# Kernel optimization log

Hardware: AMD Instinct MI355X
Metric: run time of the kernel (lower is better)

## Reference

```python
import jax, jax.numpy as jnp
import numpy as np

DIM = 512; HEADS = 8; DH = 64; CHUNK = 64; DHID = DH * 4; MAX_LR = 1.0; EPS = 1e-6


def rmsnorm(x, w):
    return x * jax.lax.rsqrt(jnp.mean(x * x, axis=-1, keepdims=True) + EPS) * w


def mem_forward(params, x):
    # MemoryMLP(depth=2, expansion=4) wrapped in ResidualNorm
    nw, w0, w1 = params
    h = rmsnorm(x, nw)
    y = jax.nn.gelu(h @ w0) @ w1
    return y + x


def chunk_loss(params, k, lr, v):
    pred = mem_forward(params, k)            # (CHUNK, DH)
    loss = jnp.mean((pred - v) ** 2, axis=-1)  # per-token mse, (CHUNK,)
    return (loss * lr).sum(), loss


def assoc_scan(gates, inputs, prev=None):
    # h_t = g_t * h_{t-1} + x_t along axis=1 (chunks)
    def combine(a, b):
        g1, x1 = a; g2, x2 = b
        return g1 * g2, x2 + g2 * x1
    G, X = jax.lax.associative_scan(combine, (gates, inputs), axis=1)
    if prev is None:
        return X
    return X + G * prev[:, None]


def setup_inputs() -> dict:
    key = jax.random.key(0)
    ks = jax.random.split(key, 8)
    B, N = 2, 4096
    s = 0.02
    return {
        'seq': jax.random.normal(ks[0], (B, N, DIM), jnp.float32),
        'store_norm_w': jnp.ones((DIM,), jnp.float32),
        'Wk': jax.random.normal(ks[1], (DIM, HEADS * DH), jnp.float32) * s,
        'Wv': jax.random.normal(ks[2], (DIM, HEADS * DH), jnp.float32) * s,
        'Wstep': jax.random.normal(ks[3], (DIM, HEADS), jnp.float32) * s,
        'bstep': jnp.zeros((HEADS,), jnp.float32),
        'Wmom': jax.random.normal(ks[4], (DIM, HEADS), jnp.float32) * s,
        'bmom': jnp.zeros((HEADS,), jnp.float32),
        'Wdec': jax.random.normal(ks[5], (DIM, HEADS), jnp.float32) * s,
        'bdec': jnp.zeros((HEADS,), jnp.float32),
        'mem_norm_w': jnp.ones((HEADS, DH), jnp.float32),
        'mem_w0': jax.random.normal(ks[6], (HEADS, DH, DHID), jnp.float32) * s,
        'mem_w1': jax.random.normal(ks[7], (HEADS, DHID, DH), jnp.float32) * s,
    }


def reference(seq, store_norm_w, Wk, Wv, Wstep, bstep, Wmom, bmom, Wdec, bdec, mem_norm_w, mem_w0, mem_w1):
    B, N, _ = seq.shape
    nc = N // CHUNK
    bh = B * HEADS
    x = rmsnorm(seq, store_norm_w)                        # store pre-norm, (B,N,D)
    # per-token adaptive lr: 'b n h -> (b h) n', sigmoid * max_lr
    lr = jax.nn.sigmoid(x @ Wstep + bstep) * MAX_LR       # (B,N,H)
    lr = lr.transpose(0, 2, 1).reshape(bh, nc, CHUNK)
    # chunk-pooled rep (AveragePool) -> momentum / decay gates per chunk
    pooled = x.reshape(B, nc, CHUNK, DIM).mean(axis=2)    # (B,nc,D)
    mom = jax.nn.sigmoid(pooled @ Wmom + bmom).transpose(0, 2, 1).reshape(bh, nc, 1)
    decay = jax.nn.sigmoid(pooled @ Wdec + bdec).transpose(0, 2, 1).reshape(bh, nc, 1)

    def split(t):  # (B,N,H*DH) -> (bh, nc, CHUNK, DH)
        return t.reshape(B, N, HEADS, DH).transpose(0, 2, 1, 3).reshape(bh, nc, CHUNK, DH)
    k = split(x @ Wk)
    v = split(x @ Wv)

    # initial fast weights per (b h) stream: repeat 'h ... -> (b h) ...'
    params0 = (jnp.tile(mem_norm_w, (B, 1)),
               jnp.tile(mem_w0, (B, 1, 1)),
               jnp.tile(mem_w1, (B, 1, 1)))

    # per-chunk per-stream grads via vmap(grad) (all chunks share the initial weights)
    grad_fn = jax.grad(chunk_loss, has_aux=True)
    per_chunk = jax.vmap(grad_fn, in_axes=(None, 0, 0, 0))
    per_bh = jax.vmap(per_chunk, in_axes=(0, 0, 0, 0))
    grads, _ = per_bh(params0, k, lr, v)                  # tuple of (bh, nc, *shape)

    finals = []
    for g, w0 in zip(grads, params0):
        surprise = -g
        extra = (1,) * (g.ndim - 2)
        m = mom.reshape(bh, nc, *extra)
        d = decay.reshape(bh, nc, *extra)
        update = assoc_scan(m, surprise)                  # momentum scan, zero init
        wts = assoc_scan(1.0 - d, update, prev=w0)        # decay recurrence from init weights
        finals.append(wts[:, -1].reshape(bh, -1))
    return jnp.concatenate(finals, axis=-1)              # (bh, DH + DH*DHID + DHID*DH)
```

## Files before the change

kernel.cpp:

```cpp
#include <hip/hip_runtime.h>
#include <math.h>

typedef __attribute__((ext_vector_type(8)))  __bf16 bf16x8;
typedef __attribute__((ext_vector_type(4)))  float  f32x4;
typedef __attribute__((ext_vector_type(4)))  unsigned short ushort4v;
typedef __attribute__((ext_vector_type(8)))  unsigned short ushort8v;

#define MFMA16(acc, a, b) acc = __builtin_amdgcn_mfma_f32_16x16x32_bf16((a),(b),(acc),0,0,0)

__device__ inline unsigned short f2b(float f) {
    union { float f; unsigned int u; } v; v.f = f;
    unsigned int r = v.u + 0x7FFFu + ((v.u >> 16) & 1u);
    return (unsigned short)(r >> 16);
}
__device__ inline float b2f(unsigned short h) {
    union { unsigned int u; float f; } v; v.u = ((unsigned int)h) << 16;
    return v.f;
}
__device__ inline float tanh_fast(float z) {
    float e = __expf(2.0f * z);
    return 1.0f - 2.0f / (e + 1.0f);
}
__device__ inline float gelu_g(float x) {
    const float c0 = 0.7978845608028654f, c1 = 0.044715f;
    float z = c0 * x * (1.0f + c1 * x * x);
    return 0.5f * x * (1.0f + tanh_fast(z));
}
__device__ inline void gelu_both(float x, float& g, float& gp) {
    const float c0 = 0.7978845608028654f, c1 = 0.044715f;
    float x2 = x * x;
    float z  = c0 * x * (1.0f + c1 * x2);
    float t  = tanh_fast(z);
    g  = 0.5f * x * (1.0f + t);
    float dz = c0 * (1.0f + 3.0f * c1 * x2);
    gp = 0.5f * (1.0f + t) + 0.5f * x * (1.0f - t * t) * dz;
}
__device__ inline float sigmoidf(float x) { return 1.0f / (1.0f + __expf(-x)); }

__global__ __launch_bounds__(256) void k_wprep(
    const float* __restrict__ Wk, const float* __restrict__ Wv,
    const float* __restrict__ w0_g, const float* __restrict__ w1_g,
    const float* __restrict__ nw_g,
    unsigned short* __restrict__ WkvT, unsigned short* __restrict__ w0fT,
    unsigned short* __restrict__ w1T, unsigned short* __restrict__ w0N,
    unsigned short* __restrict__ w1N)
{
    const int bid = blockIdx.x, tid = threadIdx.x;
    __shared__ float tile[64][65];
    if (bid < 128) {
        int kt = bid >> 4, nt = bid & 15;
        const float* src = (nt < 8) ? Wk : Wv;
        int ncol0 = (nt & 7) * 64;
        for (int ii = 0; ii < 16; ++ii) {
            int idx = tid + ii * 256; int r = idx >> 6, cc = idx & 63;
            tile[r][cc] = src[(size_t)(kt * 64 + r) * 512 + ncol0 + cc];
        }
        __syncthreads();
        for (int ii = 0; ii < 16; ++ii) {
            int idx = tid + ii * 256; int r = idx >> 6, cc = idx & 63;
            WkvT[(size_t)(nt * 64 + r) * 512 + kt * 64 + cc] = f2b(tile[cc][r]);
        }
    } else if (bid < 160) {
        int q = bid - 128; int hh = q >> 2, it = q & 3;
        const float* w0h = w0_g + hh * 16384;
        for (int ii = 0; ii < 16; ++ii) {
            int idx = tid + ii * 256; int r = idx >> 6, cc = idx & 63;
            tile[r][cc] = w0h[r * 256 + it * 64 + cc];
        }
        __syncthreads();
        for (int ii = 0; ii < 16; ++ii) {
            int idx = tid + ii * 256; int r = idx >> 6, cc = idx & 63;
            w0fT[hh * 16384 + (it * 64 + r) * 64 + cc] = f2b(nw_g[hh * 64 + cc] * tile[cc][r]);
        }
    } else if (bid < 192) {
        int q = bid - 160; int hh = q >> 2, it = q & 3;
        const float* w1h = w1_g + hh * 16384;
        for (int ii = 0; ii < 16; ++ii) {
            int idx = tid + ii * 256; int r = idx >> 6, cc = idx & 63;
            tile[r][cc] = w1h[(it * 64 + r) * 64 + cc];
        }
        __syncthreads();
        for (int ii = 0; ii < 16; ++ii) {
            int idx = tid + ii * 256; int r = idx >> 6, cc = idx & 63;
            w1T[hh * 16384 + r * 256 + it * 64 + cc] = f2b(tile[cc][r]);
        }
    } else {
        int q = bid - 192;
        int gid = q * 2048 + tid * 8;
        const float* s; unsigned short* d;
        if (gid < 131072) { s = w0_g + gid; d = w0N + gid; }
        else              { s = w1_g + (gid - 131072); d = w1N + (gid - 131072); }
        #pragma unroll
        for (int jj = 0; jj < 8; ++jj) d[jj] = f2b(s[jj]);
    }
}

__global__ __launch_bounds__(256) void k_rms_lr(
    const float* __restrict__ seq, const float* __restrict__ wnorm,
    const float* __restrict__ Wstep, const float* __restrict__ bstep,
    unsigned short* __restrict__ xb, float* __restrict__ lrb)
{
    const int wid = threadIdx.x >> 6, lane = threadIdx.x & 63;
    const int t = blockIdx.x * 4 + wid;
    const float* row = seq + (size_t)t * 512 + lane * 8;
    float v[8];
    *(f32x4*)&v[0] = *(const f32x4*)row;
    *(f32x4*)&v[4] = *(const f32x4*)(row + 4);
    float ss = 0.f;
    #pragma unroll
    for (int j = 0; j < 8; ++j) ss += v[j] * v[j];
    #pragma unroll
    for (int o = 1; o < 64; o <<= 1) ss += __shfl_xor(ss, o);
    float rr = rsqrtf(ss * (1.0f / 512.0f) + 1e-6f);
    const float* wn = wnorm + lane * 8;
    ushort8v xs;
    float acc[8] = {0.f,0.f,0.f,0.f,0.f,0.f,0.f,0.f};
    #pragma unroll
    for (int j = 0; j < 8; ++j) {
        float xf = v[j] * rr * wn[j];
        xs[j] = f2b(xf);
        const float* wrow = Wstep + (size_t)(lane * 8 + j) * 8;
        #pragma unroll
        for (int h = 0; h < 8; ++h) acc[h] = fmaf(xf, wrow[h], acc[h]);
    }
    *(ushort8v*)(xb + (size_t)t * 512 + lane * 8) = xs;
    #pragma unroll
    for (int h = 0; h < 8; ++h) {
        #pragma unroll
        for (int o = 1; o < 64; o <<= 1) acc[h] += __shfl_xor(acc[h], o);
    }
    if (lane == 0) {
        #pragma unroll
        for (int h = 0; h < 8; ++h) lrb[(size_t)t * 8 + h] = sigmoidf(acc[h] + bstep[h]);
    }
}

__global__ __launch_bounds__(256) void k_pool(
    const unsigned short* __restrict__ xb, float* __restrict__ pooled)
{
    __shared__ float sP[4][512];
    const int bc = blockIdx.x, tid = threadIdx.x;
    const int q = tid >> 6, lane = tid & 63, d0 = lane * 8;
    float p[8] = {0.f,0.f,0.f,0.f,0.f,0.f,0.f,0.f};
    for (int tt = 0; tt < 16; ++tt) {
        int t = q * 16 + tt;
        ushort8v v = *(const ushort8v*)(xb + (size_t)(bc * 64 + t) * 512 + d0);
        #pragma unroll
        for (int j = 0; j < 8; ++j) p[j] += b2f(v[j]);
    }
    #pragma unroll
    for (int j = 0; j < 8; ++j) sP[q][d0 + j] = p[j];
    __syncthreads();
    #pragma unroll
    for (int half = 0; half < 2; ++half) {
        int d = tid + half * 256;
        pooled[(size_t)bc * 512 + d] =
            (sP[0][d] + sP[1][d] + sP[2][d] + sP[3][d]) * (1.0f / 64.0f);
    }
}

__global__ __launch_bounds__(256) void k_proj(
    const unsigned short* __restrict__ xb, const unsigned short* __restrict__ WkvT,
    unsigned short* __restrict__ kbh, unsigned short* __restrict__ vb)
{
    __shared__ __attribute__((aligned(16))) unsigned short As[128][72];
    __shared__ __attribute__((aligned(16))) unsigned short Bs[128][72];
    const int tid = threadIdx.x;
    const int bm = blockIdx.x >> 3, bn = blockIdx.x & 7;
    const int m0 = bm * 128, n0 = bn * 128;
    const int wid = tid >> 6, lane = tid & 63, lg = lane >> 4, lo = lane & 15;
    const int wm = wid >> 1, wn = wid & 1;
    f32x4 acc[4][4];
    #pragma unroll
    for (int i = 0; i < 4; ++i)
        #pragma unroll
        for (int j = 0; j < 4; ++j) acc[i][j] = (f32x4)0.f;

    for (int k0 = 0; k0 < 512; k0 += 64) {
        #pragma unroll
        for (int ii = 0; ii < 4; ++ii) {
            int e0 = tid * 32 + ii * 8;
            int r = e0 >> 6, c = e0 & 63;
            *(bf16x8*)&As[r][c] = *(const bf16x8*)(xb   + (size_t)(m0 + r) * 512 + k0 + c);
            *(bf16x8*)&Bs[r][c] = *(const bf16x8*)(WkvT + (size_t)(n0 + r) * 512 + k0 + c);
        }
        __syncthreads();
        #pragma unroll
        for (int ks = 0; ks < 2; ++ks) {
            bf16x8 aF[4], bF[4];
            #pragma unroll
            for (int mt = 0; mt < 4; ++mt) aF[mt] = *(const bf16x8*)&As[wm * 64 + mt * 16 + lo][ks * 32 + 8 * lg];
            #pragma unroll
            for (int nt = 0; nt < 4; ++nt) bF[nt] = *(const bf16x8*)&Bs[wn * 64 + nt * 16 + lo][ks * 32 + 8 * lg];
            #pragma unroll
            for (int mt = 0; mt < 4; ++mt)
                #pragma unroll
                for (int nt = 0; nt < 4; ++nt) MFMA16(acc[mt][nt], aF[mt], bF[nt]);
        }
        __syncthreads();
    }
    #pragma unroll
    for (int mt = 0; mt < 4; ++mt)
        #pragma unroll
        for (int nt = 0; nt < 4; ++nt)
            #pragma unroll
            for (int r = 0; r < 4; ++r) {
                int row = m0 + wm * 64 + mt * 16 + lg * 4 + r;
                int col = n0 + wn * 64 + nt * 16 + lo;
                unsigned short val = f2b(acc[mt][nt][r]);
                if (col < 512) kbh[(size_t)row * 512 + col] = val;
                else           vb[(size_t)row * 512 + col - 512] = val;
            }
}

__global__ __launch_bounds__(64) void k_gates(
    const float* __restrict__ pooled,
    const float* __restrict__ Wmom, const float* __restrict__ bmom,
    const float* __restrict__ Wdec, const float* __restrict__ bdec,
    float* __restrict__ momout, float* __restrict__ decout)
{
    const int bc = blockIdx.x;
    const int tid = threadIdx.x, h = tid & 7, d0 = tid >> 3;
    const float* pr = pooled + (size_t)bc * 512;
    float pm = 0.f, pd = 0.f;
    #pragma unroll 8
    for (int it = 0; it < 64; ++it) {
        int d = d0 + it * 8; float pv = pr[d];
        pm = fmaf(pv, Wmom[d * 8 + h], pm);
        pd = fmaf(pv, Wdec[d * 8 + h], pd);
    }
    #pragma unroll
    for (int o = 8; o < 64; o <<= 1) { pm += __shfl_xor(pm, o); pd += __shfl_xor(pd, o); }
    if (tid < 8) {
        momout[(size_t)bc * 8 + h] = sigmoidf(pm + bmom[h]);
        decout[(size_t)bc * 8 + h] = sigmoidf(pd + bdec[h]);
    }
}

__global__ void k_coeff(const float* __restrict__ mom, const float* __restrict__ dec,
                        float* __restrict__ coeff, float* __restrict__ Aout)
{
    int s = threadIdx.x;
    if (s >= 16) return;
    int b = s >> 3, h = s & 7;
    float P = 1.f, S = 1.f;
    coeff[s * 64 + 63] = 1.f;
    for (int cc = 62; cc >= 0; --cc) {
        float Dn = 1.f - dec[(size_t)(b * 64 + cc + 1) * 8 + h];
        float Mn = mom[(size_t)(b * 64 + cc + 1) * 8 + h];
        P *= Dn;
        S = P + Mn * S;
        coeff[s * 64 + cc] = S;
    }
    float D0 = 1.f - dec[(size_t)(b * 64) * 8 + h];
    Aout[s] = P * D0;
}

__global__ __launch_bounds__(256) void k_fwd(
    const unsigned short* __restrict__ kbh, const unsigned short* __restrict__ vb,
    const float* __restrict__ lrb, const float* __restrict__ cfb,
    const unsigned short* __restrict__ w0fT, const unsigned short* __restrict__ w1T,
    unsigned short* __restrict__ uws, unsigned short* __restrict__ ews,
    unsigned short* __restrict__ ewsT)
{
    __shared__ __attribute__((aligned(16))) unsigned short sU[64][72];
    __shared__ __attribute__((aligned(16))) unsigned short sG[64][72];
    const int tid = threadIdx.x, blk = blockIdx.x;
    const int s = blk >> 6, c = blk & 63;
    const int b = s >> 3, h = s & 7;
    const int row0 = b * 4096 + c * 64;
    const int wid = tid >> 6, lane = tid & 63, lg = lane >> 4, lo = lane & 15;
    const size_t ubase = (size_t)blk * 4096;

    for (int tt = 0; tt < 16; ++tt) {
        int t = wid * 16 + tt;
        float kv = b2f(kbh[(size_t)(row0 + t) * 512 + h * 64 + lane]);
        float ss = kv * kv;
        #pragma unroll
        for (int o = 1; o < 64; o <<= 1) ss += __shfl_xor(ss, o);
        float rr = rsqrtf(ss * (1.0f / 64.0f) + 1e-6f);
        sU[t][lane] = f2b(kv * rr);
    }
    __syncthreads();
    {
        int r = tid >> 2, c0 = (tid & 3) * 16;
        *(ushort8v*)(uws + ubase + r * 64 + c0)     = *(const ushort8v*)&sU[r][c0];
        *(ushort8v*)(uws + ubase + r * 64 + c0 + 8) = *(const ushort8v*)&sU[r][c0 + 8];
    }

    const unsigned short* w0h = w0fT + h * 16384;
    const unsigned short* w1h = w1T  + h * 16384;
    bf16x8 aF0 = *(const bf16x8*)&sU[wid * 16 + lo][8 * lg];
    bf16x8 aF1 = *(const bf16x8*)&sU[wid * 16 + lo][32 + 8 * lg];

    f32x4 yac[4];
    #pragma unroll
    for (int nt = 0; nt < 4; ++nt) yac[nt] = (f32x4)0.f;

    for (int is = 0; is < 4; ++is) {
        f32x4 a1[4];
        #pragma unroll
        for (int nt = 0; nt < 4; ++nt) a1[nt] = (f32x4)0.f;
        #pragma unroll
        for (int nt = 0; nt < 4; ++nt) {
            bf16x8 b0 = *(const bf16x8*)(w0h + (size_t)(is * 64 + nt * 16 + lo) * 64 + 8 * lg);
            bf16x8 b1 = *(const bf16x8*)(w0h + (size_t)(is * 64 + nt * 16 + lo) * 64 + 32 + 8 * lg);
            MFMA16(a1[nt], aF0, b0);
            MFMA16(a1[nt], aF1, b1);
        }
        if (is > 0) __syncthreads();
        #pragma unroll
        for (int nt = 0; nt < 4; ++nt)
            #pragma unroll
            for (int r = 0; r < 4; ++r) {
                int t = wid * 16 + lg * 4 + r;
                sG[t][nt * 16 + lo] = f2b(gelu_g(a1[nt][r]));
            }
        __syncthreads();
        #pragma unroll
        for (int ks = 0; ks < 2; ++ks) {
            bf16x8 aW = *(const bf16x8*)(w1h + (size_t)(wid * 16 + lo) * 256 + is * 64 + ks * 32 + 8 * lg);
            #pragma unroll
            for (int nt = 0; nt < 4; ++nt) {
                bf16x8 bG = *(const bf16x8*)&sG[nt * 16 + lo][ks * 32 + 8 * lg];
                MFMA16(yac[nt], aW, bG);
            }
        }
    }

    float coefv = cfb[s * 64 + c];
    ushort4v evs[4];
    #pragma unroll
    for (int nt = 0; nt < 4; ++nt) {
        int t = nt * 16 + lo; int grow = row0 + t;
        float sc = -coefv * lrb[(size_t)grow * 8 + h] * (2.0f / 64.0f);
        ushort4v k4 = *(const ushort4v*)(kbh + (size_t)grow * 512 + h * 64 + wid * 16 + lg * 4);
        ushort4v v4 = *(const ushort4v*)(vb  + (size_t)grow * 512 + h * 64 + wid * 16 + lg * 4);
        ushort4v ev;
        #pragma unroll
        for (int r = 0; r < 4; ++r)
            ev[r] = f2b(sc * (yac[nt][r] + b2f(k4[r]) - b2f(v4[r])));
        evs[nt] = ev;
        *(ushort4v*)(ews + ubase + t * 64 + wid * 16 + lg * 4) = ev;
    }

    __syncthreads();
    #pragma unroll
    for (int nt = 0; nt < 4; ++nt)
        *(ushort4v*)&sG[nt * 16 + lo][wid * 16 + lg * 4] = evs[nt];
    __syncthreads();
    {
        int r2 = tid >> 2, c2 = (tid & 3) * 16;
        ushort8v o0, o1;
        #pragma unroll
        for (int jj = 0; jj < 8; ++jj) o0[jj] = sG[c2 + jj][r2];
        #pragma unroll
        for (int jj = 0; jj < 8; ++jj) o1[jj] = sG[c2 + 8 + jj][r2];
        *(ushort8v*)(ewsT + ubase + r2 * 64 + c2)     = o0;
        *(ushort8v*)(ewsT + ubase + r2 * 64 + c2 + 8) = o1;
    }
}

__global__ __launch_bounds__(256) void k_bwd(
    const unsigned short* __restrict__ uws, const unsigned short* __restrict__ ews,
    const unsigned short* __restrict__ ewsT,
    const unsigned short* __restrict__ w0fT, const unsigned short* __restrict__ w0N,
    const unsigned short* __restrict__ w1N, const float* __restrict__ nw_g,
    float* __restrict__ pws, float* __restrict__ gnwb)
{
    __shared__ __attribute__((aligned(16))) unsigned short sGT[64][72];
    __shared__ __attribute__((aligned(16))) unsigned short sDAT[64][72];
    __shared__ __attribute__((aligned(16))) unsigned short sDAN[64][68];
    const int tid = threadIdx.x, blk = blockIdx.x;
    const int s = blk >> 5, ksl = (blk >> 2) & 7, is = blk & 3;
    const int h = s & 7;
    const int wid = tid >> 6, lane = tid & 63, lg = lane >> 4, lo = lane & 15;

    f32x4 gw1a[4], gw0a[4];
    #pragma unroll
    for (int nt = 0; nt < 4; ++nt) { gw1a[nt] = (f32x4)0.f; gw0a[nt] = (f32x4)0.f; }
    float gnwp[4] = {0.f, 0.f, 0.f, 0.f};

    const unsigned short* w0fh = w0fT + h * 16384;
    const unsigned short* w0nh = w0N  + h * 16384;
    const unsigned short* w1nh = w1N  + h * 16384;

    for (int tt = 0; tt < 8; ++tt) {
        __syncthreads();
        const int chunk = ksl * 8 + tt;
        const size_t base = (size_t)(s * 64 + chunk) * 4096;

        unsigned short utg[16];
        #pragma unroll
        for (int ks = 0; ks < 2; ++ks)
            #pragma unroll
            for (int jj = 0; jj < 8; ++jj)
                utg[ks * 8 + jj] = uws[base + (size_t)(ks * 32 + 8 * lg + jj) * 64 + wid * 16 + lo];

        f32x4 a1[4];
        #pragma unroll
        for (int nt = 0; nt < 4; ++nt) a1[nt] = (f32x4)0.f;
        bf16x8 aF0 = *(const bf16x8*)(uws + base + (size_t)(wid * 16 + lo) * 64 + 8 * lg);
        bf16x8 aF1 = *(const bf16x8*)(uws + base + (size_t)(wid * 16 + lo) * 64 + 32 + 8 * lg);
        #pragma unroll
        for (int nt = 0; nt < 4; ++nt) {
            bf16x8 b0 = *(const bf16x8*)(w0fh + (size_t)(is * 64 + nt * 16 + lo) * 64 + 8 * lg);
            bf16x8 b1 = *(const bf16x8*)(w0fh + (size_t)(is * 64 + nt * 16 + lo) * 64 + 32 + 8 * lg);
            MFMA16(a1[nt], aF0, b0);
            MFMA16(a1[nt], aF1, b1);
        }
        float gpv[4][4];
        #pragma unroll
        for (int nt = 0; nt < 4; ++nt) {
            ushort4v gv;
            #pragma unroll
            for (int r = 0; r < 4; ++r) {
                float g, gp; gelu_both(a1[nt][r], g, gp);
                gv[r] = f2b(g); gpv[nt][r] = gp;
            }
            *(ushort4v*)&sGT[nt * 16 + lo][wid * 16 + lg * 4] = gv;
        }

        f32x4 dga[4];
        #pragma unroll
        for (int nt = 0; nt < 4; ++nt) dga[nt] = (f32x4)0.f;
        bf16x8 eF0 = *(const bf16x8*)(ews + base + (size_t)(wid * 16 + lo) * 64 + 8 * lg);
        bf16x8 eF1 = *(const bf16x8*)(ews + base + (size_t)(wid * 16 + lo) * 64 + 32 + 8 * lg);
        #pragma unroll
        for (int nt = 0; nt < 4; ++nt) {
            bf16x8 b0 = *(const bf16x8*)(w1nh + (size_t)(is * 64 + nt * 16 + lo) * 64 + 8 * lg);
            bf16x8 b1 = *(const bf16x8*)(w1nh + (size_t)(is * 64 + nt * 16 + lo) * 64 + 32 + 8 * lg);
            MFMA16(dga[nt], eF0, b0);
            MFMA16(dga[nt], eF1, b1);
        }
        #pragma unroll
        for (int nt = 0; nt < 4; ++nt) {
            ushort4v dv;
            #pragma unroll
            for (int r = 0; r < 4; ++r) dv[r] = f2b(dga[nt][r] * gpv[nt][r]);
            *(ushort4v*)&sDAT[nt * 16 + lo][wid * 16 + lg * 4] = dv;
            #pragma unroll
            for (int r = 0; r < 4; ++r) sDAN[wid * 16 + lg * 4 + r][nt * 16 + lo] = dv[r];
        }
        __syncthreads();

        #pragma unroll
        for (int ks = 0; ks < 2; ++ks) {
            bf16x8 aG = *(const bf16x8*)&sGT[wid * 16 + lo][ks * 32 + 8 * lg];
            #pragma unroll
            for (int nt = 0; nt < 4; ++nt) {
                bf16x8 bE = *(const bf16x8*)(ewsT + base + (size_t)(nt * 16 + lo) * 64 + ks * 32 + 8 * lg);
                MFMA16(gw1a[nt], aG, bE);
            }
        }
        #pragma unroll
        for (int ks = 0; ks < 2; ++ks) {
            union { ushort8v u; bf16x8 b; } cu;
            #pragma unroll
            for (int jj = 0; jj < 8; ++jj) cu.u[jj] = utg[ks * 8 + jj];
            #pragma unroll
            for (int nt = 0; nt < 4; ++nt) {
                bf16x8 bD = *(const bf16x8*)&sDAT[nt * 16 + lo][ks * 32 + 8 * lg];
                MFMA16(gw0a[nt], cu.b, bD);
            }
        }
        f32x4 dht[4];
        #pragma unroll
        for (int nt = 0; nt < 4; ++nt) dht[nt] = (f32x4)0.f;
        #pragma unroll
        for (int ks = 0; ks < 2; ++ks) {
            bf16x8 aW0 = *(const bf16x8*)(w0nh + (size_t)(wid * 16 + lo) * 256 + is * 64 + ks * 32 + 8 * lg);
            #pragma unroll
            for (int nt = 0; nt < 4; ++nt) {
                bf16x8 bDA = *(const bf16x8*)&sDAN[nt * 16 + lo][ks * 32 + 8 * lg];
                MFMA16(dht[nt], aW0, bDA);
            }
        }
        #pragma unroll
        for (int nt = 0; nt < 4; ++nt) {
            ushort4v u4 = *(const ushort4v*)(uws + base + (size_t)(nt * 16 + lo) * 64 + wid * 16 + lg * 4);
            #pragma unroll
            for (int r = 0; r < 4; ++r)
                gnwp[r] += b2f(u4[r]) * dht[nt][r];
        }
    }

    size_t pb = (size_t)blk * 8192;
    #pragma unroll
    for (int nt = 0; nt < 4; ++nt)
        #pragma unroll
        for (int r = 0; r < 4; ++r)
            pws[pb + (size_t)(wid * 16 + lg * 4 + r) * 64 + nt * 16 + lo] = gw1a[nt][r];
    #pragma unroll
    for (int r = 0; r < 4; ++r) {
        float nwv = nw_g[h * 64 + wid * 16 + lg * 4 + r];
        #pragma unroll
        for (int nt = 0; nt < 4; ++nt)
            pws[pb + 4096 + (size_t)(wid * 16 + lg * 4 + r) * 64 + nt * 16 + lo] = nwv * gw0a[nt][r];
    }
    #pragma unroll
    for (int r = 0; r < 4; ++r) {
        #pragma unroll
        for (int o = 1; o < 16; o <<= 1) gnwp[r] += __shfl_xor(gnwp[r], o);
    }
    if (lo == 0) {
        #pragma unroll
        for (int r = 0; r < 4; ++r)
            gnwb[(size_t)blk * 64 + wid * 16 + lg * 4 + r] = gnwp[r];
    }
}

__global__ __launch_bounds__(256) void k_reduce(
    const float* __restrict__ pws, const float* __restrict__ gnwb,
    const float* __restrict__ Ab,
    const float* __restrict__ nw_g, const float* __restrict__ w0_g,
    const float* __restrict__ w1_g, float* __restrict__ out)
{
    int gid = blockIdx.x * 256 + threadIdx.x;
    if (gid >= 16 * 32832) return;
    int s = gid / 32832, r = gid % 32832;
    int h = s & 7;
    float A = Ab[s];
    float val;
    if (r < 64) {
        val = A * nw_g[h * 64 + r];
        #pragma unroll
        for (int ks = 0; ks < 8; ++ks)
            #pragma unroll
            for (int i2 = 0; i2 < 4; ++i2)
                val += gnwb[(size_t)(s * 32 + ks * 4 + i2) * 64 + r];
    } else if (r < 16448) {
        int rr = r - 64; int d = rr >> 8; int i = rr & 255; int i2 = i >> 6, iloc = i & 63;
        val = A * w0_g[h * 16384 + rr];
        #pragma unroll
        for (int ks = 0; ks < 8; ++ks)
            val += pws[(size_t)(s * 32 + ks * 4 + i2) * 8192 + 4096 + d * 64 + iloc];
    } else {
        int rr = r - 16448; int i = rr >> 6; int j = rr & 63; int i2 = i >> 6, iloc = i & 63;
        val = A * w1_g[h * 16384 + rr];
        #pragma unroll
        for (int ks = 0; ks < 8; ++ks)
            val += pws[(size_t)(s * 32 + ks * 4 + i2) * 8192 + iloc * 64 + j];
    }
    out[gid] = val;
}

extern "C" void kernel_launch(void* const* d_in, const int* in_sizes, int n_in,
                              void* d_out, int out_size, void* d_ws, size_t ws_size,
                              hipStream_t stream) {
    (void)in_sizes; (void)n_in; (void)out_size; (void)ws_size;
    const float* seq   = (const float*)d_in[0];
    const float* snw   = (const float*)d_in[1];
    const float* Wk    = (const float*)d_in[2];
    const float* Wv    = (const float*)d_in[3];
    const float* Wstep = (const float*)d_in[4];
    const float* bstep = (const float*)d_in[5];
    const float* Wmom  = (const float*)d_in[6];
    const float* bmom  = (const float*)d_in[7];
    const float* Wdec  = (const float*)d_in[8];
    const float* bdec  = (const float*)d_in[9];
    const float* nw_g  = (const float*)d_in[10];
    const float* w0_g  = (const float*)d_in[11];
    const float* w1_g  = (const float*)d_in[12];
    float* out = (float*)d_out;

    char* ws = (char*)d_ws;
    unsigned short* xb   = (unsigned short*)(ws + 0);
    unsigned short* uws  = (unsigned short*)(ws + 0);
    unsigned short* WkvT = (unsigned short*)(ws + 8388608);
    float*          gnwb = (float*)        (ws + 8388608);
    unsigned short* kbh  = (unsigned short*)(ws + 9437184);
    unsigned short* vb   = (unsigned short*)(ws + 17825792);
    float*          pws  = (float*)        (ws + 9437184);
    unsigned short* ews  = (unsigned short*)(ws + 26214400);
    unsigned short* ewsT = (unsigned short*)(ws + 34603008);
    unsigned short* w0fT = (unsigned short*)(ws + 42991616);
    unsigned short* w1T  = (unsigned short*)(ws + 43253760);
    unsigned short* w0N  = (unsigned short*)(ws + 43515904);
    unsigned short* w1N  = (unsigned short*)(ws + 43778048);
    float* lrb  = (float*)(ws + 44040192);
    float* plb  = (float*)(ws + 44302336);
    float* momb = (float*)(ws + 44564480);
    float* decb = (float*)(ws + 44568576);
    float* cfb  = (float*)(ws + 44572672);
    float* Ab   = (float*)(ws + 44576768);

    k_wprep <<<320, 256, 0, stream>>>(Wk, Wv, w0_g, w1_g, nw_g, WkvT, w0fT, w1T, w0N, w1N);
    k_rms_lr<<<2048, 256, 0, stream>>>(seq, snw, Wstep, bstep, xb, lrb);
    k_pool  <<<128, 256, 0, stream>>>(xb, plb);
    k_proj  <<<512, 256, 0, stream>>>(xb, WkvT, kbh, vb);
    k_gates <<<128, 64, 0, stream>>>(plb, Wmom, bmom, Wdec, bdec, momb, decb);
    k_coeff <<<1, 64, 0, stream>>>(momb, decb, cfb, Ab);
    k_fwd   <<<1024, 256, 0, stream>>>(kbh, vb, lrb, cfb, w0fT, w1T, uws, ews, ewsT);
    k_bwd   <<<512, 256, 0, stream>>>(uws, ews, ewsT, w0fT, w0N, w1N, nw_g, pws, gnwb);
    k_reduce<<<2052, 256, 0, stream>>>(pws, gnwb, Ab, nw_g, w0_g, w1_g, out);
}
```

Before: 152.5 us.

## Replace partial-sum reduce kernel with atomic accumulation and split backward finer

After: 177.8 us. +16.6%, slower.

```diff
diff --git a/kernel.cpp b/kernel.cpp
--- a/kernel.cpp
+++ b/kernel.cpp
@@ -256,6 +256,22 @@
     Aout[s] = P * D0;
 }
 
+__global__ __launch_bounds__(256) void k_init_out(
+    const float* __restrict__ nw_g, const float* __restrict__ w0_g,
+    const float* __restrict__ w1_g, const float* __restrict__ Aout,
+    float* __restrict__ out)
+{
+    int gid = blockIdx.x * 256 + threadIdx.x;
+    if (gid >= 16 * 32832) return;
+    int s = gid / 32832, r = gid % 32832;
+    int h = s & 7;
+    float v;
+    if (r < 64)          v = nw_g[h * 64 + r];
+    else if (r < 16448)  v = w0_g[h * 16384 + (r - 64)];
+    else                 v = w1_g[h * 16384 + (r - 16448)];
+    out[gid] = Aout[s] * v;
+}
+
 __global__ __launch_bounds__(256) void k_fwd(
     const unsigned short* __restrict__ kbh, const unsigned short* __restrict__ vb,
     const float* __restrict__ lrb, const float* __restrict__ cfb,
@@ -272,21 +288,29 @@
     const int wid = tid >> 6, lane = tid & 63, lg = lane >> 4, lo = lane & 15;
     const size_t ubase = (size_t)blk * 4096;
 
-    for (int tt = 0; tt < 16; ++tt) {
-        int t = wid * 16 + tt;
-        float kv = b2f(kbh[(size_t)(row0 + t) * 512 + h * 64 + lane]);
-        float ss = kv * kv;
-        #pragma unroll
-        for (int o = 1; o < 64; o <<= 1) ss += __shfl_xor(ss, o);
-        float rr = rsqrtf(ss * (1.0f / 64.0f) + 1e-6f);
-        sU[t][lane] = f2b(kv * rr);
-    }
-    __syncthreads();
     {
         int r = tid >> 2, c0 = (tid & 3) * 16;
-        *(ushort8v*)(uws + ubase + r * 64 + c0)     = *(const ushort8v*)&sU[r][c0];
-        *(ushort8v*)(uws + ubase + r * 64 + c0 + 8) = *(const ushort8v*)&sU[r][c0 + 8];
-    }
+        const unsigned short* kr = kbh + (size_t)(row0 + r) * 512 + h * 64 + c0;
+        ushort8v k0 = *(const ushort8v*)kr;
+        ushort8v k1 = *(const ushort8v*)(kr + 8);
+        float kv[16];
+        float ss = 0.f;
+        #pragma unroll
+        for (int j = 0; j < 8; ++j) { kv[j] = b2f(k0[j]); kv[8 + j] = b2f(k1[j]); }
+        #pragma unroll
+        for (int j = 0; j < 16; ++j) ss += kv[j] * kv[j];
+        ss += __shfl_xor(ss, 1);
+        ss += __shfl_xor(ss, 2);
+        float rr = rsqrtf(ss * (1.0f / 64.0f) + 1e-6f);
+        ushort8v u0, u1;
+        #pragma unroll
+        for (int j = 0; j < 8; ++j) { u0[j] = f2b(kv[j] * rr); u1[j] = f2b(kv[8 + j] * rr); }
+        *(ushort8v*)&sU[r][c0]     = u0;
+        *(ushort8v*)&sU[r][c0 + 8] = u1;
+        *(ushort8v*)(uws + ubase + r * 64 + c0)     = u0;
+        *(ushort8v*)(uws + ubase + r * 64 + c0 + 8) = u1;
+    }
+    __syncthreads();
 
     const unsigned short* w0h = w0fT + h * 16384;
     const unsigned short* w1h = w1T  + h * 16384;
@@ -366,13 +390,13 @@
     const unsigned short* __restrict__ ewsT,
     const unsigned short* __restrict__ w0fT, const unsigned short* __restrict__ w0N,
     const unsigned short* __restrict__ w1N, const float* __restrict__ nw_g,
-    float* __restrict__ pws, float* __restrict__ gnwb)
+    float* __restrict__ out)
 {
     __shared__ __attribute__((aligned(16))) unsigned short sGT[64][72];
     __shared__ __attribute__((aligned(16))) unsigned short sDAT[64][72];
     __shared__ __attribute__((aligned(16))) unsigned short sDAN[64][68];
     const int tid = threadIdx.x, blk = blockIdx.x;
-    const int s = blk >> 5, ksl = (blk >> 2) & 7, is = blk & 3;
+    const int s = blk >> 6, ksl = (blk >> 2) & 15, is = blk & 3;
     const int h = s & 7;
     const int wid = tid >> 6, lane = tid & 63, lg = lane >> 4, lo = lane & 15;
 
@@ -385,9 +409,9 @@
     const unsigned short* w0nh = w0N  + h * 16384;
     const unsigned short* w1nh = w1N  + h * 16384;
 
-    for (int tt = 0; tt < 8; ++tt) {
-        __syncthreads();
-        const int chunk = ksl * 8 + tt;
+    for (int tt = 0; tt < 4; ++tt) {
+        __syncthreads();
+        const int chunk = ksl * 4 + tt;
         const size_t base = (size_t)(s * 64 + chunk) * 4096;
 
         unsigned short utg[16];
@@ -485,64 +509,32 @@
         }
     }
 
-    size_t pb = (size_t)blk * 8192;
+    float* outS = out + (size_t)s * 32832;
     #pragma unroll
     for (int nt = 0; nt < 4; ++nt)
         #pragma unroll
+        for (int r = 0; r < 4; ++r) {
+            int iglob = is * 64 + wid * 16 + lg * 4 + r;
+            atomicAdd(outS + 16448 + iglob * 64 + nt * 16 + lo, gw1a[nt][r]);
+        }
+    #pragma unroll
+    for (int r = 0; r < 4; ++r) {
+        int d = wid * 16 + lg * 4 + r;
+        float nwv = nw_g[h * 64 + d];
+        #pragma unroll
+        for (int nt = 0; nt < 4; ++nt)
+            atomicAdd(outS + 64 + d * 256 + is * 64 + nt * 16 + lo, nwv * gw0a[nt][r]);
+    }
+    #pragma unroll
+    for (int r = 0; r < 4; ++r) {
+        #pragma unroll
+        for (int o = 1; o < 16; o <<= 1) gnwp[r] += __shfl_xor(gnwp[r], o);
+    }
+    if (lo == 0) {
+        #pragma unroll
         for (int r = 0; r < 4; ++r)
-            pws[pb + (size_t)(wid * 16 + lg * 4 + r) * 64 + nt * 16 + lo] = gw1a[nt][r];
-    #pragma unroll
-    for (int r = 0; r < 4; ++r) {
-        float nwv = nw_g[h * 64 + wid * 16 + lg * 4 + r];
-        #pragma unroll
-        for (int nt = 0; nt < 4; ++nt)
-            pws[pb + 4096 + (size_t)(wid * 16 + lg * 4 + r) * 64 + nt * 16 + lo] = nwv * gw0a[nt][r];
-    }
-    #pragma unroll
-    for (int r = 0; r < 4; ++r) {
-        #pragma unroll
-        for (int o = 1; o < 16; o <<= 1) gnwp[r] += __shfl_xor(gnwp[r], o);
-    }
-    if (lo == 0) {
-        #pragma unroll
-        for (int r = 0; r < 4; ++r)
-            gnwb[(size_t)blk * 64 + wid * 16 + lg * 4 + r] = gnwp[r];
-    }
-}
-
-__global__ __launch_bounds__(256) void k_reduce(
-    const float* __restrict__ pws, const float* __restrict__ gnwb,
-    const float* __restrict__ Ab,
-    const float* __restrict__ nw_g, const float* __restrict__ w0_g,
-    const float* __restrict__ w1_g, float* __restrict__ out)
-{
-    int gid = blockIdx.x * 256 + threadIdx.x;
-    if (gid >= 16 * 32832) return;
-    int s = gid / 32832, r = gid % 32832;
-    int h = s & 7;
-    float A = Ab[s];
-    float val;
-    if (r < 64) {
-        val = A * nw_g[h * 64 + r];
-        #pragma unroll
-        for (int ks = 0; ks < 8; ++ks)
-            #pragma unroll
-            for (int i2 = 0; i2 < 4; ++i2)
-                val += gnwb[(size_t)(s * 32 + ks * 4 + i2) * 64 + r];
-    } else if (r < 16448) {
-        int rr = r - 64; int d = rr >> 8; int i = rr & 255; int i2 = i >> 6, iloc = i & 63;
-        val = A * w0_g[h * 16384 + rr];
-        #pragma unroll
-        for (int ks = 0; ks < 8; ++ks)
-            val += pws[(size_t)(s * 32 + ks * 4 + i2) * 8192 + 4096 + d * 64 + iloc];
-    } else {
-        int rr = r - 16448; int i = rr >> 6; int j = rr & 63; int i2 = i >> 6, iloc = i & 63;
-        val = A * w1_g[h * 16384 + rr];
-        #pragma unroll
-        for (int ks = 0; ks < 8; ++ks)
-            val += pws[(size_t)(s * 32 + ks * 4 + i2) * 8192 + iloc * 64 + j];
-    }
-    out[gid] = val;
+            atomicAdd(outS + wid * 16 + lg * 4 + r, gnwp[r]);
+    }
 }
 
 extern "C" void kernel_launch(void* const* d_in, const int* in_sizes, int n_in,
@@ -568,10 +560,8 @@
     unsigned short* xb   = (unsigned short*)(ws + 0);
     unsigned short* uws  = (unsigned short*)(ws + 0);
     unsigned short* WkvT = (unsigned short*)(ws + 8388608);
-    float*          gnwb = (float*)        (ws + 8388608);
     unsigned short* kbh  = (unsigned short*)(ws + 9437184);
     unsigned short* vb   = (unsigned short*)(ws + 17825792);
-    float*          pws  = (float*)        (ws + 9437184);
     unsigned short* ews  = (unsigned short*)(ws + 26214400);
     unsigned short* ewsT = (unsigned short*)(ws + 34603008);
     unsigned short* w0fT = (unsigned short*)(ws + 42991616);
@@ -585,13 +575,13 @@
     float* cfb  = (float*)(ws + 44572672);
     float* Ab   = (float*)(ws + 44576768);
 
-    k_wprep <<<320, 256, 0, stream>>>(Wk, Wv, w0_g, w1_g, nw_g, WkvT, w0fT, w1T, w0N, w1N);
-    k_rms_lr<<<2048, 256, 0, stream>>>(seq, snw, Wstep, bstep, xb, lrb);
-    k_pool  <<<128, 256, 0, stream>>>(xb, plb);
-    k_proj  <<<512, 256, 0, stream>>>(xb, WkvT, kbh, vb);
-    k_gates <<<128, 64, 0, stream>>>(plb, Wmom, bmom, Wdec, bdec, momb, decb);
-    k_coeff <<<1, 64, 0, stream>>>(momb, decb, cfb, Ab);
-    k_fwd   <<<1024, 256, 0, stream>>>(kbh, vb, lrb, cfb, w0fT, w1T, uws, ews, ewsT);
-    k_bwd   <<<512, 256, 0, stream>>>(uws, ews, ewsT, w0fT, w0N, w1N, nw_g, pws, gnwb);
-    k_reduce<<<2052, 256, 0, stream>>>(pws, gnwb, Ab, nw_g, w0_g, w1_g, out);
-}
+    k_wprep   <<<320, 256, 0, stream>>>(Wk, Wv, w0_g, w1_g, nw_g, WkvT, w0fT, w1T, w0N, w1N);
+    k_rms_lr  <<<2048, 256, 0, stream>>>(seq, snw, Wstep, bstep, xb, lrb);
+    k_pool    <<<128, 256, 0, stream>>>(xb, plb);
+    k_proj    <<<512, 256, 0, stream>>>(xb, WkvT, kbh, vb);
+    k_gates   <<<128, 64, 0, stream>>>(plb, Wmom, bmom, Wdec, bdec, momb, decb);
+    k_coeff   <<<1, 64, 0, stream>>>(momb, decb, cfb, Ab);
+    k_init_out<<<2052, 256, 0, stream>>>(nw_g, w0_g, w1_g, Ab, out);
+    k_fwd     <<<1024, 256, 0, stream>>>(kbh, vb, lrb, cfb, w0fT, w1T, uws, ews, ewsT);
+    k_bwd     <<<1024, 256, 0, stream>>>(uws, ews, ewsT, w0fT, w0N, w1N, nw_g, out);
+}
```
